# Optimization experiments

Hardware: AMD Instinct MI355X
Metric: run time of the kernel (lower is better)

## Reference

```python
import jax, jax.numpy as jnp
import numpy as np

B, S, D = 2, 2048, 2048
H, HKV = 32, 8
HD = D // H  # 64
NEG_INF = -1e9


def _rope_tables(seq_len, head_dim):
    inv_freq = 1.0 / (10000.0 ** (np.arange(0, head_dim, 2, dtype=np.float32) / head_dim))
    t = np.arange(seq_len, dtype=np.float32)
    freqs = np.outer(t, inv_freq)                      # (S, HD/2)
    emb = np.concatenate([freqs, freqs], axis=-1)      # (S, HD)
    cos = np.cos(emb)[None, None]                      # (1,1,S,HD)
    sin = np.sin(emb)[None, None]
    return jnp.asarray(cos), jnp.asarray(sin)


def setup_inputs() -> dict:
    key = jax.random.key(0)
    ks = jax.random.split(key, 5)
    hidden_states = jax.random.normal(ks[0], (B, S, D), dtype=jnp.float32)
    # causal additive mask: 0 where allowed, -inf (large negative) where masked
    causal = jnp.tril(jnp.ones((S, S), dtype=jnp.bool_))
    attention_mask = jnp.where(causal, 0.0, NEG_INF).astype(jnp.float32)
    attention_mask = jnp.broadcast_to(attention_mask[None, None], (B, 1, S, S))
    cos, sin = _rope_tables(S, HD)
    sc = 0.02
    Wq = jax.random.normal(ks[1], (D, H * HD), dtype=jnp.float32) * sc
    Wk = jax.random.normal(ks[2], (D, HKV * HD), dtype=jnp.float32) * sc
    Wv = jax.random.normal(ks[3], (D, HKV * HD), dtype=jnp.float32) * sc
    Wo = jax.random.normal(ks[4], (H * HD, D), dtype=jnp.float32) * sc
    return {"hidden_states": hidden_states, "attention_mask": attention_mask,
            "cos": cos, "sin": sin, "Wq": Wq, "Wk": Wk, "Wv": Wv, "Wo": Wo}


def _rotate_half(x):
    x1, x2 = jnp.split(x, 2, axis=-1)
    return jnp.concatenate([-x2, x1], axis=-1)


def _apply_rope(x, cos, sin):
    # x: (B, h, S, HD); cos/sin: (1,1,S,HD)
    return x * cos + _rotate_half(x) * sin


def reference(hidden_states, attention_mask, cos, sin, Wq, Wk, Wv, Wo):
    b, s, _ = hidden_states.shape
    scale = 1.0 / np.sqrt(HD)
    q = (hidden_states @ Wq).reshape(b, s, H, HD).transpose(0, 2, 1, 3)    # (B,H,S,HD)
    k = (hidden_states @ Wk).reshape(b, s, HKV, HD).transpose(0, 2, 1, 3)  # (B,HKV,S,HD)
    v = (hidden_states @ Wv).reshape(b, s, HKV, HD).transpose(0, 2, 1, 3)
    q = _apply_rope(q, cos, sin)
    k = _apply_rope(k, cos, sin)
    # GQA: group query heads per kv head without materializing repeated KV
    g = H // HKV
    qg = q.reshape(b, HKV, g, s, HD)
    scores = jnp.einsum('bkgqd,bksd->bkgqs', qg, k) * scale               # (B,HKV,g,S,S)
    scores = scores + attention_mask[:, :, None]                          # broadcast (B,1,1,S,S)
    attn = jax.nn.softmax(scores, axis=-1)
    out = jnp.einsum('bkgqs,bksd->bkgqd', attn, v)                        # (B,HKV,g,S,HD)
    out = out.reshape(b, H, s, HD).transpose(0, 2, 1, 3).reshape(b, s, H * HD)
    return out @ Wo
```

## Files before the change

kernel.cpp:

```cpp
#include <hip/hip_runtime.h>
#include <math.h>

typedef _Float16 half8 __attribute__((ext_vector_type(8)));
typedef _Float16 half4 __attribute__((ext_vector_type(4)));
typedef _Float16 half2 __attribute__((ext_vector_type(2)));
typedef float f32x4 __attribute__((ext_vector_type(4)));

#define S_LEN 2048
#define DM    2048
#define NH    32
#define NKV   8

#define QSCALE 0.1803368801111204f
#define NSHIFT -11.541560327111707f

#if __has_builtin(__builtin_amdgcn_exp2f)
#define EXP2(x) __builtin_amdgcn_exp2f(x)
#else
#define EXP2(x) __builtin_exp2f(x)
#endif

__device__ __forceinline__ half2 pkrtz(float a, float b) {
    return __builtin_bit_cast(half2, __builtin_amdgcn_cvt_pkrtz(a, b));
}

__device__ __forceinline__ void async16(const void* g, void* l) {
    __builtin_amdgcn_global_load_lds(
        (const __attribute__((address_space(1))) unsigned int*)g,
        (__attribute__((address_space(3))) unsigned int*)l, 16, 0, 0);
}

__global__ __launch_bounds__(256) void prep_all(
    const float* __restrict__ Wq, const float* __restrict__ Wk,
    const float* __restrict__ Wv, const float* __restrict__ Wo,
    const float* __restrict__ hidden,
    _Float16* __restrict__ Wqkv_t, _Float16* __restrict__ Wo_t,
    _Float16* __restrict__ hid_h)
{
    const int z = blockIdx.z;
    if (z == 4) {
        const size_t i = ((size_t)(blockIdx.y * 64 + blockIdx.x) * 256 + threadIdx.x) * 8;
        float4 v0 = *(const float4*)(hidden + i);
        float4 v1 = *(const float4*)(hidden + i + 4);
        half8 o = {(_Float16)v0.x, (_Float16)v0.y, (_Float16)v0.z, (_Float16)v0.w,
                   (_Float16)v1.x, (_Float16)v1.y, (_Float16)v1.z, (_Float16)v1.w};
        *(half8*)(hid_h + i) = o;
        return;
    }
    const float* W; _Float16* Wt; int N;
    if (z == 0)      { W = Wq; Wt = Wqkv_t;                        N = 2048; }
    else if (z == 1) { W = Wk; Wt = Wqkv_t + (size_t)2048 * 2048;  N = 512;  }
    else if (z == 2) { W = Wv; Wt = Wqkv_t + (size_t)2560 * 2048;  N = 512;  }
    else             { W = Wo; Wt = Wo_t;                          N = 2048; }
    if ((int)blockIdx.x * 32 >= N) return;

    __shared__ float t[32][33];
    const int n0 = blockIdx.x * 32, k0 = blockIdx.y * 32;
    const int tx = threadIdx.x & 31, ty = threadIdx.x >> 5;
#pragma unroll
    for (int i = 0; i < 32; i += 8)
        t[ty + i][tx] = W[(size_t)(k0 + ty + i) * N + n0 + tx];
    __syncthreads();
#pragma unroll
    for (int i = 0; i < 32; i += 8)
        Wt[(size_t)(n0 + ty + i) * 2048 + k0 + tx] = (_Float16)t[tx][ty + i];
}

__global__ __launch_bounds__(256, 3) void gemm_h(
    const _Float16* __restrict__ A, const _Float16* __restrict__ Bt,
    void* __restrict__ Cout, int N, int K, int mode,
    const float* __restrict__ cosT, const float* __restrict__ sinT)
{
    __shared__ __align__(16) _Float16 Al[128 * 64];
    __shared__ __align__(16) _Float16 Bl[128 * 64];
    const int tid  = threadIdx.x;
    const int lane = tid & 63;
    const int wave = tid >> 6;
    const int lm = lane & 15, quad = lane >> 4;
    const int wm = wave >> 1;
    const int wn = wave & 1;

    const int gx  = gridDim.x;
    const int nwg = gx * gridDim.y;
    const int lin = blockIdx.y * gx + blockIdx.x;
    const int tsw = (lin & 7) * (nwg >> 3) + (lin >> 3);
    const int bm  = (tsw / gx) * 128, bn = (tsw % gx) * 128;
    const int nt  = K >> 6;

    const int r8   = tid >> 3;
    const int gcol = ((tid & 7) ^ (r8 & 7)) << 3;
    const _Float16* pA = A  + (size_t)(bm + r8) * K + gcol;
    const _Float16* pB = Bt + (size_t)(bn + r8) * K + gcol;
    char* ldsA = (char*)Al + tid * 16;
    char* ldsB = (char*)Bl + tid * 16;

#define STAGE(t) do {                                                     \
        const int ko_ = (t) * 64;                                         \
        _Pragma("unroll")                                                 \
        for (int u_ = 0; u_ < 4; ++u_) {                                  \
            async16(pA + (size_t)(u_ * 32) * K + ko_, ldsA + u_ * 4096);  \
            async16(pB + (size_t)(u_ * 32) * K + ko_, ldsB + u_ * 4096);  \
        }                                                                 \
    } while (0)

    const int cs0 = ((quad       ^ (lm & 7)) << 3);
    const int cs1 = (((4 + quad) ^ (lm & 7)) << 3);
    const _Float16* Arow = Al + (wm * 64 + lm) * 64;
    const _Float16* Brow = Bl + (wn * 64 + lm) * 64;

    f32x4 acc[4][4];
#pragma unroll
    for (int i = 0; i < 4; ++i)
#pragma unroll
        for (int j = 0; j < 4; ++j) acc[i][j] = (f32x4){0.f, 0.f, 0.f, 0.f};

#define MFMA16()                                                              \
    _Pragma("unroll") for (int i_ = 0; i_ < 4; ++i_)                          \
    _Pragma("unroll") for (int j_ = 0; j_ < 4; ++j_)                          \
        acc[i_][j_] = __builtin_amdgcn_mfma_f32_16x16x32_f16(                 \
            af[i_], bf[j_], acc[i_][j_], 0, 0, 0);

    STAGE(0);
    for (int kt = 0; kt < nt; ++kt) {
        asm volatile("s_waitcnt vmcnt(0)" ::: "memory");
        __builtin_amdgcn_s_barrier();
        half8 af[4], bf[4];
#pragma unroll
        for (int i = 0; i < 4; ++i) af[i] = *(const half8*)(Arow + i * 1024 + cs0);
#pragma unroll
        for (int j = 0; j < 4; ++j) bf[j] = *(const half8*)(Brow + j * 1024 + cs0);
        MFMA16();
#pragma unroll
        for (int i = 0; i < 4; ++i) af[i] = *(const half8*)(Arow + i * 1024 + cs1);
#pragma unroll
        for (int j = 0; j < 4; ++j) bf[j] = *(const half8*)(Brow + j * 1024 + cs1);
        MFMA16();
        __builtin_amdgcn_s_barrier();
        if (kt + 1 < nt) STAGE(kt + 1);
    }
#undef STAGE
#undef MFMA16

    const int mrowq = bm + wm * 64 + (quad << 2);
    if (mode == 0) {
        float* C = (float*)Cout;
        const int col0 = bn + wn * 64 + lm;
#pragma unroll
        for (int mf = 0; mf < 4; ++mf)
#pragma unroll
            for (int r = 0; r < 4; ++r) {
                const int m = mrowq + mf * 16 + r;
#pragma unroll
                for (int nf = 0; nf < 4; ++nf)
                    C[(size_t)m * N + col0 + nf * 16] = acc[mf][nf][r];
            }
        return;
    }

    _Float16* Cq = (_Float16*)Cout;
    _Float16* Ck = Cq + (size_t)2 * NH * S_LEN * 64;
    _Float16* Cv = Ck + (size_t)2 * NKV * S_LEN * 64;
    const int colbase = bn + wn * 64;
    const int region = (colbase >= 2560) ? 2 : (colbase >= 2048) ? 1 : 0;

    if (region == 2) {
        const int head = (colbase - 2560) >> 6;
#pragma unroll
        for (int mf = 0; mf < 4; ++mf) {
            const int m0 = mrowq + mf * 16;
            const int b = m0 >> 11, s0 = m0 & 2047;
#pragma unroll
            for (int nf = 0; nf < 4; ++nf) {
                half2 lo = pkrtz(acc[mf][nf][0], acc[mf][nf][1]);
                half2 hi = pkrtz(acc[mf][nf][2], acc[mf][nf][3]);
                half4 ov = {lo[0], lo[1], hi[0], hi[1]};
                *(half4*)(Cv + ((((size_t)b * NKV + head) << 6) + lm + nf * 16) * S_LEN + s0) = ov;
            }
        }
        return;
    }

    const float qscale = (region == 0) ? QSCALE : 1.0f;
    const int head = (region == 0) ? (colbase >> 6) : ((colbase - 2048) >> 6);
    _Float16* Cdst = (region == 0) ? Cq : Ck;
    const int nh = (region == 0) ? NH : NKV;
#pragma unroll
    for (int mf = 0; mf < 4; ++mf)
#pragma unroll
        for (int r = 0; r < 4; ++r) {
            int m = mrowq + mf * 16 + r;
            int b = m >> 11, s = m & 2047;
            const float c0 = cosT[s * 64 + lm], c16 = cosT[s * 64 + lm + 16];
            const float s0 = sinT[s * 64 + lm], s16 = sinT[s * 64 + lm + 16];
            float a0r = acc[mf][0][r], a1r = acc[mf][1][r];
            float a2r = acc[mf][2][r], a3r = acc[mf][3][r];
            float o0 = (a0r * c0  - a2r * s0)  * qscale;
            float o1 = (a1r * c16 - a3r * s16) * qscale;
            float o2 = (a2r * c0  + a0r * s0)  * qscale;
            float o3 = (a3r * c16 + a1r * s16) * qscale;
            _Float16* d = Cdst + ((((size_t)b * nh + head) * S_LEN + s) << 6) + lm;
            d[0]  = (_Float16)o0;
            d[16] = (_Float16)o1;
            d[32] = (_Float16)o2;
            d[48] = (_Float16)o3;
        }
}

#define LSWOFS(row, halfofs) \
    ((row) * 64 + (((((halfofs) >> 3) & 7) ^ ((row) & 7)) << 3) + ((halfofs) & 7))

__global__ __launch_bounds__(256, 2) void attn_h(
    const _Float16* __restrict__ q, const _Float16* __restrict__ k,
    const _Float16* __restrict__ vt, _Float16* __restrict__ x2)
{
    __shared__ __align__(16) _Float16 Ks[2][64 * 64];
    __shared__ __align__(16) _Float16 Vts[2][64 * 64];

    const int tid = threadIdx.x;
    const int wave = tid >> 6, lane = tid & 63;
    const int lm = lane & 15, quad = lane >> 4;

    const int lin = ((int)blockIdx.z * 8 + (int)blockIdx.y) * 64 + (int)blockIdx.x;
    const int tsw = (lin & 7) * 128 + (lin >> 3);
    const int qt  = 63 - (tsw & 63);
    const int kvh = (tsw >> 6) & 7;
    const int b   = tsw >> 9;
    const int h   = kvh * 4 + wave;
    const int ktm = (qt * 32 + 31) >> 6;

    const _Float16* kbase  = k  + ((((size_t)b * NKV + kvh) * S_LEN) << 6);
    const _Float16* vtbase = vt + ((((size_t)b * NKV + kvh) << 6) * S_LEN);

    half8 qf[2][2];
    {
        const _Float16* qb = q + ((((size_t)b * NH + h) * S_LEN + qt * 32) << 6);
#pragma unroll
        for (int i = 0; i < 2; ++i)
#pragma unroll
            for (int kk = 0; kk < 2; ++kk)
                qf[i][kk] = *(const half8*)(qb + (i * 16 + lm) * 64 + kk * 32 + quad * 8);
    }

    f32x4 accOT[2][4];
    float lpart[2];
#pragma unroll
    for (int i = 0; i < 2; ++i) {
        lpart[i] = 0.f;
#pragma unroll
        for (int j = 0; j < 4; ++j) accOT[i][j] = (f32x4){0.f, 0.f, 0.f, 0.f};
    }

    const int f0 = tid * 16, f1 = 4096 + tid * 16;
    const int r0 = f0 >> 7, r1 = f1 >> 7;
    const int c0 = ((f0 >> 4) & 7) ^ (r0 & 7);
    const int c1 = ((f1 >> 4) & 7) ^ (r1 & 7);
    const char* ksrc0 = (const char*)kbase  + r0 * 128 + c0 * 16;
    const char* ksrc1 = (const char*)kbase  + r1 * 128 + c1 * 16;
    const char* vsrc0 = (const char*)vtbase + (size_t)r0 * 4096 + c0 * 16;
    const char* vsrc1 = (const char*)vtbase + (size_t)r1 * 4096 + c1 * 16;

#define STAGEKV(kt, nb) do {                                          \
        async16(ksrc0 + (size_t)(kt) * 8192, (char*)Ks[nb]  + f0);    \
        async16(ksrc1 + (size_t)(kt) * 8192, (char*)Ks[nb]  + f1);    \
        async16(vsrc0 + (kt) * 128,          (char*)Vts[nb] + f0);    \
        async16(vsrc1 + (kt) * 128,          (char*)Vts[nb] + f1);    \
    } while (0)

    STAGEKV(0, 0);
    asm volatile("s_waitcnt vmcnt(0)" ::: "memory");
    __builtin_amdgcn_s_barrier();

    for (int kt = 0; kt <= ktm; ++kt) {
        const int cur = kt & 1;
        if (kt < ktm) STAGEKV(kt + 1, cur ^ 1);
        const _Float16* Kc = Ks[cur];
        const _Float16* Vc = Vts[cur];

        half8 kf[4][2];
        half4 vtf[4][4];
#pragma unroll
        for (int t = 0; t < 4; ++t) {
#pragma unroll
            for (int kk = 0; kk < 2; ++kk)
                kf[t][kk] = *(const half8*)(Kc + LSWOFS(t * 16 + lm, kk * 32 + quad * 8));
#pragma unroll
            for (int j = 0; j < 4; ++j)
                vtf[j][t] = *(const half4*)(Vc + LSWOFS(j * 16 + lm, t * 16 + quad * 4));
        }

        const bool diag = (kt == ktm);
#pragma unroll
        for (int i = 0; i < 2; ++i) {
            f32x4 sc[4];
            __builtin_amdgcn_s_setprio(1);
#pragma unroll
            for (int t = 0; t < 4; ++t) {
                f32x4 z = (f32x4){NSHIFT, NSHIFT, NSHIFT, NSHIFT};
                z = __builtin_amdgcn_mfma_f32_16x16x32_f16(kf[t][0], qf[i][0], z, 0, 0, 0);
                z = __builtin_amdgcn_mfma_f32_16x16x32_f16(kf[t][1], qf[i][1], z, 0, 0, 0);
                sc[t] = z;
            }
            __builtin_amdgcn_s_setprio(0);
            if (diag) {
                const int qpos = qt * 32 + i * 16 + lm;
#pragma unroll
                for (int t = 0; t < 4; ++t)
#pragma unroll
                    for (int r = 0; r < 4; ++r) {
                        int key = kt * 64 + t * 16 + quad * 4 + r;
                        if (key > qpos) sc[t][r] = -30000.f;
                    }
            }
            half4 pt[4];
            float lp = 0.f;
#pragma unroll
            for (int t = 0; t < 4; ++t) {
                float p0 = EXP2(sc[t][0]), p1 = EXP2(sc[t][1]);
                float p2 = EXP2(sc[t][2]), p3 = EXP2(sc[t][3]);
                lp += (p0 + p1) + (p2 + p3);
                half2 lo = pkrtz(p0, p1);
                half2 hi = pkrtz(p2, p3);
                pt[t] = (half4){lo[0], lo[1], hi[0], hi[1]};
            }
            lpart[i] += lp;
            __builtin_amdgcn_s_setprio(1);
#pragma unroll
            for (int j = 0; j < 4; ++j)
#pragma unroll
                for (int t = 0; t < 4; ++t)
                    accOT[i][j] = __builtin_amdgcn_mfma_f32_16x16x16f16(
                        vtf[j][t], pt[t], accOT[i][j], 0, 0, 0);
            __builtin_amdgcn_s_setprio(0);
        }
        asm volatile("s_waitcnt vmcnt(0)" ::: "memory");
        __builtin_amdgcn_s_barrier();
    }
#undef STAGEKV

#pragma unroll
    for (int i = 0; i < 2; ++i) {
        float l = lpart[i];
        l += __shfl_xor(l, 16);
        l += __shfl_xor(l, 32);
        const float inv = 1.f / l;
        const size_t row = (size_t)b * S_LEN + qt * 32 + i * 16 + lm;
#pragma unroll
        for (int j = 0; j < 4; ++j) {
            f32x4 o = accOT[i][j];
            half2 lo = pkrtz(o[0] * inv, o[1] * inv);
            half2 hi = pkrtz(o[2] * inv, o[3] * inv);
            half4 ov = {lo[0], lo[1], hi[0], hi[1]};
            *(half4*)(x2 + row * DM + h * 64 + j * 16 + quad * 4) = ov;
        }
    }
}

extern "C" void kernel_launch(void* const* d_in, const int* in_sizes, int n_in,
                              void* d_out, int out_size, void* d_ws, size_t ws_size,
                              hipStream_t stream)
{
    const float* hidden = (const float*)d_in[0];
    const float* cosT = (const float*)d_in[2];
    const float* sinT = (const float*)d_in[3];
    const float* Wq = (const float*)d_in[4];
    const float* Wk = (const float*)d_in[5];
    const float* Wv = (const float*)d_in[6];
    const float* Wo = (const float*)d_in[7];
    float* out = (float*)d_out;

    _Float16* w = (_Float16*)d_ws;
    _Float16* hid_h  = w;  w += (size_t)4096 * 2048;
    _Float16* Wqkv_t = w;  w += (size_t)3072 * 2048;
    _Float16* Wo_t   = w;  w += (size_t)2048 * 2048;
    _Float16* qh     = w;  w += (size_t)2 * NH * S_LEN * 64;
    _Float16* kh     = w;  w += (size_t)2 * NKV * S_LEN * 64;
    _Float16* vth    = w;  w += (size_t)2 * NKV * S_LEN * 64;
    _Float16* x2h    = w;

    dim3 blk(256);
    prep_all<<<dim3(64, 64, 5), blk, 0, stream>>>(Wq, Wk, Wv, Wo, hidden,
                                                  Wqkv_t, Wo_t, hid_h);

    gemm_h<<<dim3(24, 32), blk, 0, stream>>>(hid_h, Wqkv_t, qh, 3072, 2048, 1, cosT, sinT);

    attn_h<<<dim3(64, 8, 2), blk, 0, stream>>>(qh, kh, vth, x2h);

    gemm_h<<<dim3(16, 32), blk, 0, stream>>>(x2h, Wo_t, out, 2048, 2048, 0, nullptr, nullptr);
}
```

Before: 299.7 us.

## Split GEMM K-tile into two halves and overlap async loads with MFMA

The GEMM main loop now splits each 64-wide K tile into two 32-wide LDS halves with a new swizzle. Loads for the next tile's first half are issued while the current second half is being computed, and likewise for the other half. This is meant to hide global-to-LDS latency behind MFMA work instead of waiting on a full-tile barrier each iteration. It adds more barriers and finer vmcnt accounting, and the tighter synchronization could cost throughput if latency is not actually the bottleneck.

```diff
diff --git a/kernel.cpp b/kernel.cpp
--- a/kernel.cpp
+++ b/kernel.cpp
@@ -71,8 +71,8 @@
     void* __restrict__ Cout, int N, int K, int mode,
     const float* __restrict__ cosT, const float* __restrict__ sinT)
 {
-    __shared__ __align__(16) _Float16 Al[128 * 64];
-    __shared__ __align__(16) _Float16 Bl[128 * 64];
+    __shared__ __align__(16) _Float16 Al[2 * 128 * 32];
+    __shared__ __align__(16) _Float16 Bl[2 * 128 * 32];
     const int tid  = threadIdx.x;
     const int lane = tid & 63;
     const int wave = tid >> 6;
@@ -87,26 +87,22 @@
     const int bm  = (tsw / gx) * 128, bn = (tsw % gx) * 128;
     const int nt  = K >> 6;
 
-    const int r8   = tid >> 3;
-    const int gcol = ((tid & 7) ^ (r8 & 7)) << 3;
-    const _Float16* pA = A  + (size_t)(bm + r8) * K + gcol;
-    const _Float16* pB = Bt + (size_t)(bn + r8) * K + gcol;
-    char* ldsA = (char*)Al + tid * 16;
-    char* ldsB = (char*)Bl + tid * 16;
-
-#define STAGE(t) do {                                                     \
-        const int ko_ = (t) * 64;                                         \
-        _Pragma("unroll")                                                 \
-        for (int u_ = 0; u_ < 4; ++u_) {                                  \
-            async16(pA + (size_t)(u_ * 32) * K + ko_, ldsA + u_ * 4096);  \
-            async16(pB + (size_t)(u_ * 32) * K + ko_, ldsB + u_ * 4096);  \
-        }                                                                 \
-    } while (0)
-
-    const int cs0 = ((quad       ^ (lm & 7)) << 3);
-    const int cs1 = (((4 + quad) ^ (lm & 7)) << 3);
-    const _Float16* Arow = Al + (wm * 64 + lm) * 64;
-    const _Float16* Brow = Bl + (wn * 64 + lm) * 64;
+    const int t4 = tid >> 2;
+    const int lg = (((tid & 3) ^ ((t4 >> 1) & 3)) << 3);
+    const _Float16* pA = A  + (size_t)(bm + t4) * K + lg;
+    const _Float16* pB = Bt + (size_t)(bn + t4) * K + lg;
+
+#define STAGEH(t, kh) do { if ((t) < nt) {                                 \
+        const int co_ = (t) * 64 + (kh) * 32;                              \
+        char* dA_ = (char*)Al + (kh) * 8192 + tid * 16;                    \
+        char* dB_ = (char*)Bl + (kh) * 8192 + tid * 16;                    \
+        async16(pA + co_, dA_);  async16(pA + (size_t)64 * K + co_, dA_ + 4096); \
+        async16(pB + co_, dB_);  async16(pB + (size_t)64 * K + co_, dB_ + 4096); \
+    } } while (0)
+
+    const int csw = ((quad ^ ((lm >> 1) & 3)) << 3);
+    const _Float16* Arow = Al + (wm * 64 + lm) * 32 + csw;
+    const _Float16* Brow = Bl + (wn * 64 + lm) * 32 + csw;
 
     f32x4 acc[4][4];
 #pragma unroll
@@ -120,25 +116,34 @@
         acc[i_][j_] = __builtin_amdgcn_mfma_f32_16x16x32_f16(                 \
             af[i_], bf[j_], acc[i_][j_], 0, 0, 0);
 
-    STAGE(0);
+    STAGEH(0, 0); STAGEH(0, 1);
+    asm volatile("s_waitcnt vmcnt(4)" ::: "memory");
+    __builtin_amdgcn_s_barrier();
+
     for (int kt = 0; kt < nt; ++kt) {
-        asm volatile("s_waitcnt vmcnt(0)" ::: "memory");
+        const bool more = (kt + 1) < nt;
+        half8 af[4], bf[4];
+#pragma unroll
+        for (int i = 0; i < 4; ++i) af[i] = *(const half8*)(Arow + i * 512);
+#pragma unroll
+        for (int j = 0; j < 4; ++j) bf[j] = *(const half8*)(Brow + j * 512);
+        asm volatile("s_waitcnt lgkmcnt(0) vmcnt(0)" ::: "memory");
         __builtin_amdgcn_s_barrier();
-        half8 af[4], bf[4];
-#pragma unroll
-        for (int i = 0; i < 4; ++i) af[i] = *(const half8*)(Arow + i * 1024 + cs0);
-#pragma unroll
-        for (int j = 0; j < 4; ++j) bf[j] = *(const half8*)(Brow + j * 1024 + cs0);
+        STAGEH(kt + 1, 0);
         MFMA16();
 #pragma unroll
-        for (int i = 0; i < 4; ++i) af[i] = *(const half8*)(Arow + i * 1024 + cs1);
-#pragma unroll
-        for (int j = 0; j < 4; ++j) bf[j] = *(const half8*)(Brow + j * 1024 + cs1);
+        for (int i = 0; i < 4; ++i) af[i] = *(const half8*)(Arow + 4096 + i * 512);
+#pragma unroll
+        for (int j = 0; j < 4; ++j) bf[j] = *(const half8*)(Brow + 4096 + j * 512);
+        asm volatile("s_waitcnt lgkmcnt(0)" ::: "memory");
+        __builtin_amdgcn_s_barrier();
+        STAGEH(kt + 1, 1);
         MFMA16();
+        if (more) asm volatile("s_waitcnt vmcnt(4)" ::: "memory");
+        else      asm volatile("s_waitcnt vmcnt(0)" ::: "memory");
         __builtin_amdgcn_s_barrier();
-        if (kt + 1 < nt) STAGE(kt + 1);
-    }
-#undef STAGE
+    }
+#undef STAGEH
 #undef MFMA16
 
     const int mrowq = bm + wm * 64 + (quad << 2);
```

After: 301.5 us. About the same (+0.6%).
